# Performance work log

Measured on AMD Instinct MI355X. Metric: run time of the kernel, lower is better.

The kernel has to match this reference:

```python
import jax, jax.numpy as jnp
import numpy as np

EPS = 1e-5  # torch BatchNorm default eps
B, C, T, NOUT, NCLS = 4096, 32, 512, 16, 4


def setup_inputs() -> dict:
    key = jax.random.key(0)
    ks = jax.random.split(key, 12)
    s = lambda k, shape: jax.random.normal(k, shape, jnp.float32) * 0.05
    return {
        "de": jax.random.normal(ks[0], (B, C, T), jnp.float32),
        "adj": jax.random.normal(ks[1], (B, C, C), jnp.float32),  # unused by forward (module recomputes corr)
        "dw_w": s(ks[2], (C, 1, 3)),      # depthwise Conv1d weight [C,1,3]
        "dw_b": s(ks[3], (C,)),
        "pw_w": s(ks[4], (C, C)),          # pointwise 1x1 conv [out,in]
        "pw_b": s(ks[5], (C,)),
        "bn1_g": jnp.ones((C,), jnp.float32),
        "bn1_b": jnp.zeros((C,), jnp.float32),
        "gc_w": s(ks[6], (T, NOUT)),       # GraphConvolution weight
        "fc_w": s(ks[7], (C * NOUT, C)),   # fc62 Linear(512,32)
        "fc_b": s(ks[8], (C,)),
        "bn2_g": jnp.ones((C,), jnp.float32),
        "bn2_b": jnp.zeros((C,), jnp.float32),
        "cls_w": s(ks[9], (C, NCLS)),      # fcclass Linear(32,4)
        "cls_b": s(ks[10], (NCLS,)),
    }


def reference(de, adj, dw_w, dw_b, pw_w, pw_b, bn1_g, bn1_b, gc_w,
              fc_w, fc_b, bn2_g, bn2_b, cls_w, cls_b):
    # --- SeparableConv2d (really 1d): depthwise k=3 -> pointwise 1x1 -> BN -> relu ---
    x = jax.lax.conv_general_dilated(
        de, dw_w, window_strides=(1,), padding=[(1, 1)],
        dimension_numbers=("NCH", "OIH", "NCH"),
        feature_group_count=de.shape[1]) + dw_b[None, :, None]
    x = jnp.einsum("oc,bct->bot", pw_w, x) + pw_b[None, :, None]
    m = x.mean((0, 2), keepdims=True)
    v = x.var((0, 2), keepdims=True)  # biased, as BN normalization uses
    x = (x - m) / jnp.sqrt(v + EPS) * bn1_g[None, :, None] + bn1_b[None, :, None]
    x = jax.nn.relu(x)                       # [B, C, T]

    # --- batched Pearson corrcoef over the time axis (vectorizes the per-sample loop) ---
    xt = x.transpose(0, 2, 1)                # [B, T, C]
    Tn = xt.shape[1]
    f = (Tn - 1) / Tn
    xc = xt - xt.mean(1, keepdims=True)
    num = jnp.einsum("btn,btm->bnm", xc, xc) / Tn   # biased covariance
    var = xt.var(1, ddof=1)                         # torch var default unbiased
    den = jnp.sqrt(var[:, :, None] * var[:, None, :]) * f
    cor = num / den                          # [B, C, C]

    # --- Chebyshev graph convolution (single K term, adj = cor) + relu ---
    g = jnp.einsum("bnm,bmt->bnt", cor, x)   # message passing over channel graph
    g = jax.nn.relu(jnp.einsum("bnt,to->bno", g, gc_w))  # [B, C, 16]

    # --- fc62: Linear -> BN1d -> (dropout: identity) -> sigmoid ---
    h = g.reshape(g.shape[0], -1) @ fc_w + fc_b          # [B, 32]
    m2 = h.mean(0)
    v2 = h.var(0)
    h = (h - m2) / jnp.sqrt(v2 + EPS) * bn2_g + bn2_b
    h = jax.nn.sigmoid(h)

    return h @ cls_w + cls_b                 # [B, 4]
```

## Files before the change

### kernel.cpp

```cpp
#include <hip/hip_runtime.h>
#include <math.h>

#define BB 4096
#define CC 32
#define TT 512
#define NOUTC 16
#define EPSF 1e-5f
#define XS 520


typedef __attribute__((ext_vector_type(16))) float f32x16;
typedef __attribute__((ext_vector_type(4)))  float f32x4;
typedef __attribute__((ext_vector_type(8)))  short short8;
typedef __attribute__((ext_vector_type(4)))  unsigned int u32x4;
typedef __attribute__((ext_vector_type(4)))  float vf4;
typedef vf4 __attribute__((aligned(4))) vf4u;

__device__ __forceinline__ unsigned short f2b(float f) {
  unsigned int u = __builtin_bit_cast(unsigned int, f);
  return (unsigned short)((u + 0x7FFFu + ((u >> 16) & 1u)) >> 16);
}
__device__ __forceinline__ float blo(unsigned int u) {
  return __builtin_bit_cast(float, u << 16);
}
__device__ __forceinline__ float bhi(unsigned int u) {
  return __builtin_bit_cast(float, u & 0xFFFF0000u);
}

__device__ __forceinline__ void conv_cols(const float* __restrict__ deb,
    const float* __restrict__ dw, const float* __restrict__ db_,
    int tid, float* x1A, float* x1B) {
  int t0 = tid * 2;
  int off = (tid == 0) ? 0 : ((tid == 255) ? t0 - 2 : t0 - 1);
#pragma unroll
  for (int c = 0; c < CC; c++) {
    vf4u v = *reinterpret_cast<const vf4u*>(deb + c * TT + off);
    float vm1 = (tid == 0) ? 0.f : ((tid == 255) ? v.y : v.x);
    float v0  = (tid == 0) ? v.x : ((tid == 255) ? v.z : v.y);
    float vp1 = (tid == 0) ? v.y : ((tid == 255) ? v.w : v.z);
    float vp2 = (tid == 0) ? v.z : ((tid == 255) ? 0.f : v.w);
    float w0 = dw[c * 3], w1 = dw[c * 3 + 1], w2 = dw[c * 3 + 2], bc = db_[c];
    x1A[c] = fmaf(w0, vm1, fmaf(w1, v0, fmaf(w2, vp1, bc)));
    x1B[c] = fmaf(w0, v0, fmaf(w1, vp1, fmaf(w2, vp2, bc)));
  }
}

__global__ __launch_bounds__(256) void k1_stats(const float* __restrict__ de,
    const float* __restrict__ dw, const float* __restrict__ db_,
    const float* __restrict__ pw, const float* __restrict__ pwb,
    float* __restrict__ part, unsigned int* __restrict__ x2h, int useWs) {
  __shared__ float pr[4 * 64];
  int tid = threadIdx.x, b = blockIdx.x;
  int w = tid >> 6, lane = tid & 63;
  const float* deb = de + (size_t)b * CC * TT;
  float x1A[CC], x1B[CC];
  conv_cols(deb, dw, db_, tid, x1A, x1B);
  unsigned int* xw = x2h + (size_t)b * CC * 256;
#pragma unroll
  for (int o = 0; o < CC; o++) {
    float aA = pwb[o], aB = pwb[o];
#pragma unroll
    for (int c = 0; c < CC; c++) { float pv = pw[o * CC + c]; aA = fmaf(pv, x1A[c], aA); aB = fmaf(pv, x1B[c], aB); }
    if (useWs) xw[o * 256 + tid] = (unsigned int)f2b(aA) | ((unsigned int)f2b(aB) << 16);
    float s = aA + aB, q = fmaf(aA, aA, aB * aB);
#pragma unroll
    for (int d = 1; d < 64; d <<= 1) { s += __shfl_xor(s, d); q += __shfl_xor(q, d); }
    if (lane == 0) { pr[w * 64 + o] = s; pr[w * 64 + 32 + o] = q; }
  }
  __syncthreads();
  if (tid < 64) {
    part[(size_t)tid * BB + b] = pr[tid] + pr[64 + tid] + pr[128 + tid] + pr[192 + tid];
  }
}

__global__ void k2_bn1(const float* __restrict__ part, const float* __restrict__ g,
                       const float* __restrict__ bta, float* __restrict__ ws) {
  __shared__ float redS[256], redQ[256];
  int o = blockIdx.x, tid = threadIdx.x;
  const float* ps = part + (size_t)o * BB;
  const float* pq = part + (size_t)(CC + o) * BB;
  float s = 0, q = 0;
  for (int i = tid; i < BB; i += 256) { s += ps[i]; q += pq[i]; }
  redS[tid] = s; redQ[tid] = q;
  __syncthreads();
  for (int k = 128; k > 0; k >>= 1) {
    if (tid < k) { redS[tid] += redS[tid + k]; redQ[tid] += redQ[tid + k]; }
    __syncthreads();
  }
  if (tid == 0) {
    float N = (float)BB * (float)TT;
    float mean = redS[0] / N;
    float var = redQ[0] / N - mean * mean;
    float sc = g[o] / sqrtf(var + EPSF);
    ws[o] = sc;
    ws[32 + o] = bta[o] - mean * sc;
  }
}

__global__ __launch_bounds__(256) void k3_main(const float* __restrict__ de,
    const float* __restrict__ dw, const float* __restrict__ db_,
    const float* __restrict__ pw, const float* __restrict__ pwb,
    const float* __restrict__ ws, const float* __restrict__ gcw,
    const float* __restrict__ fcw, const float* __restrict__ fcb,
    float* __restrict__ hT, const unsigned int* __restrict__ x2h, int useWs) {
  __shared__ __align__(16) unsigned short x_s[CC * XS];
  __shared__ __align__(16) unsigned short gc_s[NOUTC * XS];
  __shared__ float gramP[2][CC * CC];
  __shared__ float zP[2][CC * NOUTC];
  __shared__ float num_s[CC * 33];
  __shared__ float red16[CC * 8];
  __shared__ float mu_s[CC], inv_s[CC];
  __shared__ float Zi_s[CC * NOUTC];
  __shared__ float g2_s[CC * NOUTC];
  __shared__ float red2[CC * 9];

  int tid = threadIdx.x, b = blockIdx.x;
  int w = tid >> 6, lane = tid & 63;
  int t0 = tid * 2;

  for (int i = tid; i < TT * NOUTC; i += 256) {
    int t = i >> 4, o = i & 15;
    gc_s[o * XS + t] = f2b(gcw[i]);
  }

  if (useWs) {
    const unsigned int* xr = x2h + (size_t)b * CC * 256;
#pragma unroll
    for (int o = 0; o < CC; o++) {
      unsigned int u = xr[o * 256 + tid];
      float sc = ws[o], sh = ws[32 + o];
      unsigned short hA = f2b(fmaxf(fmaf(blo(u), sc, sh), 0.f));
      unsigned short hB = f2b(fmaxf(fmaf(bhi(u), sc, sh), 0.f));
      *(unsigned int*)(&x_s[o * XS + t0]) = (unsigned int)hA | ((unsigned int)hB << 16);
    }
  } else {
    const float* deb = de + (size_t)b * CC * TT;
    float x1A[CC], x1B[CC];
    conv_cols(deb, dw, db_, tid, x1A, x1B);
#pragma unroll
    for (int o = 0; o < CC; o++) {
      float aA = pwb[o], aB = pwb[o];
#pragma unroll
      for (int c = 0; c < CC; c++) { float pv = pw[o * CC + c]; aA = fmaf(pv, x1A[c], aA); aB = fmaf(pv, x1B[c], aB); }
      float sc = ws[o], sh = ws[32 + o];
      unsigned short hA = f2b(fmaxf(fmaf(aA, sc, sh), 0.f));
      unsigned short hB = f2b(fmaxf(fmaf(aB, sc, sh), 0.f));
      *(unsigned int*)(&x_s[o * XS + t0]) = (unsigned int)hA | ((unsigned int)hB << 16);
    }
  }
  __syncthreads();

  {
    int c = tid >> 3, j = tid & 7;
    float s = 0.f;
#pragma unroll
    for (int it = 0; it < 8; it++) {
      u32x4 u = *reinterpret_cast<const u32x4*>(&x_s[c * XS + j * 64 + it * 8]);
#pragma unroll
      for (int k = 0; k < 4; k++) s += blo(u[k]) + bhi(u[k]);
    }
    red16[c * 8 + j] = s;
  }

  if (w < 2) {
    int m = lane & 31, kh = lane >> 5;
    f32x16 acc;
#pragma unroll
    for (int r = 0; r < 16; r++) acc[r] = 0.f;
    int kbase = w * 256 + kh * 8;
#pragma unroll
    for (int kk = 0; kk < 256; kk += 16) {
      short8 a = *(const short8*)(&x_s[m * XS + kbase + kk]);
      acc = __builtin_amdgcn_mfma_f32_32x32x16_bf16(a, a, acc, 0, 0, 0);
    }
#pragma unroll
    for (int r = 0; r < 16; r++) {
      int row = (r & 3) + 8 * (r >> 2) + 4 * kh;
      gramP[w][row * CC + m] = acc[r];
    }
  } else {
    int w2 = w - 2;
    int n16 = lane & 15, q = lane >> 4;
    f32x4 ac0, ac1;
#pragma unroll
    for (int r = 0; r < 4; r++) { ac0[r] = 0.f; ac1[r] = 0.f; }
    int kbase = w2 * 256 + q * 8;
#pragma unroll
    for (int kk = 0; kk < 256; kk += 32) {
      short8 bfr = *(const short8*)(&gc_s[n16 * XS + kbase + kk]);
      short8 af0 = *(const short8*)(&x_s[n16 * XS + kbase + kk]);
      short8 af1 = *(const short8*)(&x_s[(16 + n16) * XS + kbase + kk]);
      ac0 = __builtin_amdgcn_mfma_f32_16x16x32_bf16(af0, bfr, ac0, 0, 0, 0);
      ac1 = __builtin_amdgcn_mfma_f32_16x16x32_bf16(af1, bfr, ac1, 0, 0, 0);
    }
#pragma unroll
    for (int r = 0; r < 4; r++) {
      int row = q * 4 + r;
      zP[w2][row * NOUTC + n16] = ac0[r];
      zP[w2][(16 + row) * NOUTC + n16] = ac1[r];
    }
  }
  __syncthreads();
  if (tid < CC) {
    float s = 0.f;
#pragma unroll
    for (int j = 0; j < 8; j++) s += red16[tid * 8 + j];
    mu_s[tid] = s;
  }
  __syncthreads();
  for (int i = tid; i < CC * CC; i += 256) {
    int n = i >> 5, m = i & 31;
    num_s[n * 33 + m] = gramP[0][i] + gramP[1][i] - mu_s[n] * mu_s[m] * (1.f / (float)TT);
  }
  for (int i = tid; i < CC * NOUTC; i += 256) Zi_s[i] = zP[0][i] + zP[1][i];
  __syncthreads();
  if (tid < CC) inv_s[tid] = rsqrtf(num_s[tid * 33 + tid]);
  __syncthreads();
  for (int i = tid; i < CC * NOUTC; i += 256) {
    int n = i >> 4, o = i & 15;
    float s = 0.f;
#pragma unroll
    for (int m = 0; m < CC; m++) s = fmaf(num_s[n * 33 + m] * inv_s[m], Zi_s[m * NOUTC + o], s);
    g2_s[i] = fmaxf(s * inv_s[n], 0.f);
  }
  __syncthreads();
  {
    int j = tid & 31, ch = tid >> 5;
    float p = 0.f;
#pragma unroll
    for (int ii = 0; ii < 64; ii++) {
      int i = ch * 64 + ii;
      p = fmaf(g2_s[i], fcw[i * CC + j], p);
    }
    red2[j * 9 + ch] = p;
  }
  __syncthreads();
  if (tid < CC) {
    float h = fcb[tid];
#pragma unroll
    for (int ch = 0; ch < 8; ch++) h += red2[tid * 9 + ch];
    hT[(size_t)tid * BB + b] = h;
  }
}

__global__ void k4_bn2(const float* __restrict__ hT, const float* __restrict__ g,
                       const float* __restrict__ bta, float* __restrict__ ws) {
  __shared__ float redS[256], redQ[256];
  int j = blockIdx.x, tid = threadIdx.x;
  const float* row = hT + (size_t)j * BB;
  float s = 0, q = 0;
  for (int i = tid; i < BB; i += 256) { float v = row[i]; s += v; q = fmaf(v, v, q); }
  redS[tid] = s; redQ[tid] = q;
  __syncthreads();
  for (int k = 128; k > 0; k >>= 1) {
    if (tid < k) { redS[tid] += redS[tid + k]; redQ[tid] += redQ[tid + k]; }
    __syncthreads();
  }
  if (tid == 0) {
    float N = (float)BB;
    float mean = redS[0] / N;
    float var = redQ[0] / N - mean * mean;
    float sc = g[j] / sqrtf(var + EPSF);
    ws[64 + j] = sc;
    ws[96 + j] = bta[j] - mean * sc;
  }
}

__global__ void k5_out(const float* __restrict__ hT, const float* __restrict__ ws,
                       const float* __restrict__ clsw, const float* __restrict__ clsb,
                       float* __restrict__ out) {
  __shared__ float hs[CC * 257];
  int b0 = blockIdx.x * 256, tid = threadIdx.x;
  for (int i = tid; i < CC * 256; i += 256) {
    int j = i >> 8, bb = i & 255;
    float v = fmaf(hT[(size_t)j * BB + b0 + bb], ws[64 + j], ws[96 + j]);
    hs[j * 257 + bb] = 1.f / (1.f + expf(-v));
  }
  __syncthreads();
  float o0 = clsb[0], o1 = clsb[1], o2 = clsb[2], o3 = clsb[3];
#pragma unroll
  for (int j = 0; j < CC; j++) {
    float h = hs[j * 257 + tid];
    o0 = fmaf(h, clsw[j * 4 + 0], o0);
    o1 = fmaf(h, clsw[j * 4 + 1], o1);
    o2 = fmaf(h, clsw[j * 4 + 2], o2);
    o3 = fmaf(h, clsw[j * 4 + 3], o3);
  }
  float4* out4 = reinterpret_cast<float4*>(out);
  out4[b0 + tid] = make_float4(o0, o1, o2, o3);
}

extern "C" void kernel_launch(void* const* d_in, const int* in_sizes, int n_in,
                              void* d_out, int out_size, void* d_ws, size_t ws_size,
                              hipStream_t stream) {
  const float* de   = (const float*)d_in[0];
  const float* dw   = (const float*)d_in[2];
  const float* db_  = (const float*)d_in[3];
  const float* pw   = (const float*)d_in[4];
  const float* pwb  = (const float*)d_in[5];
  const float* bn1g = (const float*)d_in[6];
  const float* bn1b = (const float*)d_in[7];
  const float* gcw  = (const float*)d_in[8];
  const float* fcw  = (const float*)d_in[9];
  const float* fcb  = (const float*)d_in[10];
  const float* bn2g = (const float*)d_in[11];
  const float* bn2b = (const float*)d_in[12];
  const float* clsw = (const float*)d_in[13];
  const float* clsb = (const float*)d_in[14];

  float* ws   = (float*)d_ws;
  float* hT   = ws + 128;
  float* part = ws + 131200;
  unsigned int* x2h = (unsigned int*)(ws + 393344);
  float* out  = (float*)d_out;

  size_t need = 393344ull * 4ull + (size_t)BB * CC * 256 * 4;
  int useWs = (ws_size >= need) ? 1 : 0;

  k1_stats<<<BB, 256, 0, stream>>>(de, dw, db_, pw, pwb, part, x2h, useWs);
  k2_bn1<<<CC, 256, 0, stream>>>(part, bn1g, bn1b, ws);
  k3_main<<<BB, 256, 0, stream>>>(de, dw, db_, pw, pwb, ws, gcw, fcw, fcb, hT, x2h, useWs);
  k4_bn2<<<CC, 256, 0, stream>>>(hT, bn2g, bn2b, ws);
  k5_out<<<BB / 256, 256, 0, stream>>>(hT, ws, clsw, clsb, out);
}
```

Baseline: 511.5 us.

## Compute pointwise conv in k1 with split-bf16 MFMA via LDS staging

Replaces the per-thread scalar FMA loop for the 32x32 pointwise conv in k1_stats with bf16 MFMA 32x32x16 instructions. Both operands are split into hi and lo bf16 parts, and three MFMAs per k-step keep roughly fp32 accuracy. Conv outputs are staged in LDS and the results are transposed through LDS. BN statistics are then computed from the bf16-rounded values and stored as coalesced 16-byte writes. This removes a large ALU cost, but adds LDS traffic, extra barriers, and higher LDS usage that may limit occupancy. Statistics now come from rounded values, which slightly changes numerics.

Measured after the change: 521.4 us. No clear change (+1.9%).

```diff
diff --git a/kernel.cpp b/kernel.cpp
--- a/kernel.cpp
+++ b/kernel.cpp
@@ -25,6 +25,9 @@
 }
 __device__ __forceinline__ float bhi(unsigned int u) {
   return __builtin_bit_cast(float, u & 0xFFFF0000u);
+}
+__device__ __forceinline__ unsigned int pk2(float a, float b) {
+  return (unsigned int)f2b(a) | ((unsigned int)f2b(b) << 16);
 }
 
 __device__ __forceinline__ void conv_cols(const float* __restrict__ deb,
@@ -45,31 +48,116 @@
   }
 }
 
+__device__ __forceinline__ void stage_row(unsigned short* lds1, int XHo, int XLo,
+                                          int row, const float* x) {
+#pragma unroll
+  for (int cb = 0; cb < 4; cb++) {
+    u32x4 hv, lv;
+#pragma unroll
+    for (int k = 0; k < 4; k++) {
+      float a = x[cb * 8 + 2 * k], b2 = x[cb * 8 + 2 * k + 1];
+      unsigned int ua = __builtin_bit_cast(unsigned int, a);
+      unsigned int ub = __builtin_bit_cast(unsigned int, b2);
+      hv[k] = (ua >> 16) | (ub & 0xFFFF0000u);
+      float ra = a - __builtin_bit_cast(float, ua & 0xFFFF0000u);
+      float rb = b2 - __builtin_bit_cast(float, ub & 0xFFFF0000u);
+      lv[k] = pk2(ra, rb);
+    }
+    *(u32x4*)&lds1[XHo + row * 40 + cb * 8] = hv;
+    *(u32x4*)&lds1[XLo + row * 40 + cb * 8] = lv;
+  }
+}
+
 __global__ __launch_bounds__(256) void k1_stats(const float* __restrict__ de,
     const float* __restrict__ dw, const float* __restrict__ db_,
     const float* __restrict__ pw, const float* __restrict__ pwb,
     float* __restrict__ part, unsigned int* __restrict__ x2h, int useWs) {
-  __shared__ float pr[4 * 64];
+  __shared__ __align__(16) unsigned short lds1[39168];
+  const int XHo = 0, XLo = 10240, X2Bo = 20480, PWHo = 37120, PWLo = 38144;
+
   int tid = threadIdx.x, b = blockIdx.x;
-  int w = tid >> 6, lane = tid & 63;
+  int lane = tid & 63, w = tid >> 6;
+  int m31 = lane & 31, kh = lane >> 5;
+
   const float* deb = de + (size_t)b * CC * TT;
   float x1A[CC], x1B[CC];
   conv_cols(deb, dw, db_, tid, x1A, x1B);
-  unsigned int* xw = x2h + (size_t)b * CC * 256;
-#pragma unroll
-  for (int o = 0; o < CC; o++) {
-    float aA = pwb[o], aB = pwb[o];
-#pragma unroll
-    for (int c = 0; c < CC; c++) { float pv = pw[o * CC + c]; aA = fmaf(pv, x1A[c], aA); aB = fmaf(pv, x1B[c], aB); }
-    if (useWs) xw[o * 256 + tid] = (unsigned int)f2b(aA) | ((unsigned int)f2b(aB) << 16);
-    float s = aA + aB, q = fmaf(aA, aA, aB * aB);
+
+  for (int i = tid; i < CC * CC; i += 256) {
+    float v = pw[i];
+    unsigned int u = __builtin_bit_cast(unsigned int, v);
+    lds1[PWHo + i] = (unsigned short)(u >> 16);
+    float r = v - __builtin_bit_cast(float, u & 0xFFFF0000u);
+    lds1[PWLo + i] = f2b(r);
+  }
+  __syncthreads();
+
+  short8 ah[2], al[2];
+#pragma unroll
+  for (int s = 0; s < 2; s++) {
+    ah[s] = *(const short8*)&lds1[PWHo + m31 * 32 + s * 16 + kh * 8];
+    al[s] = *(const short8*)&lds1[PWLo + m31 * 32 + s * 16 + kh * 8];
+  }
+  float pbv[16];
+#pragma unroll
+  for (int r = 0; r < 16; r++) pbv[r] = pwb[(r & 3) + 8 * (r >> 2) + 4 * kh];
+
+#pragma unroll
+  for (int h = 0; h < 2; h++) {
+    if ((tid >> 7) == h) {
+      int lr = 2 * (tid & 127);
+      stage_row(lds1, XHo, XLo, lr, x1A);
+      stage_row(lds1, XHo, XLo, lr + 1, x1B);
+    }
+    __syncthreads();
+
+#pragma unroll
+    for (int i = 0; i < 2; i++) {
+      int wt = w * 2 + i;
+      f32x16 acc;
+#pragma unroll
+      for (int r = 0; r < 16; r++) acc[r] = 0.f;
+      int rowb = wt * 32 + m31;
+#pragma unroll
+      for (int s = 0; s < 2; s++) {
+        short8 bh = *(const short8*)&lds1[XHo + rowb * 40 + s * 16 + kh * 8];
+        short8 bl = *(const short8*)&lds1[XLo + rowb * 40 + s * 16 + kh * 8];
+        acc = __builtin_amdgcn_mfma_f32_32x32x16_bf16(ah[s], bh, acc, 0, 0, 0);
+        acc = __builtin_amdgcn_mfma_f32_32x32x16_bf16(ah[s], bl, acc, 0, 0, 0);
+        acc = __builtin_amdgcn_mfma_f32_32x32x16_bf16(al[s], bh, acc, 0, 0, 0);
+      }
+      int t = h * 256 + wt * 32 + m31;
+#pragma unroll
+      for (int pr = 0; pr < 8; pr++) {
+        int o0 = ((2 * pr) & 3) + 8 * (pr >> 1) + 4 * kh;
+        unsigned int p = pk2(acc[2 * pr] + pbv[2 * pr], acc[2 * pr + 1] + pbv[2 * pr + 1]);
+        lds1[X2Bo + o0 * 520 + t] = (unsigned short)(p & 0xFFFFu);
+        lds1[X2Bo + (o0 + 1) * 520 + t] = (unsigned short)(p >> 16);
+      }
+    }
+    __syncthreads();
+  }
+
+  unsigned int* xw = x2h + (size_t)b * (CC * 256);
+  int L = tid & 63;
+#pragma unroll
+  for (int it = 0; it < 8; it++) {
+    int o = it * 4 + w;
+    u32x4 v = *(const u32x4*)&lds1[X2Bo + o * 520 + L * 8];
+    float s = 0.f, q = 0.f;
+#pragma unroll
+    for (int k = 0; k < 4; k++) {
+      float a = blo(v[k]), c2 = bhi(v[k]);
+      s += a + c2;
+      q = fmaf(a, a, fmaf(c2, c2, q));
+    }
 #pragma unroll
     for (int d = 1; d < 64; d <<= 1) { s += __shfl_xor(s, d); q += __shfl_xor(q, d); }
-    if (lane == 0) { pr[w * 64 + o] = s; pr[w * 64 + 32 + o] = q; }
-  }
-  __syncthreads();
-  if (tid < 64) {
-    part[(size_t)tid * BB + b] = pr[tid] + pr[64 + tid] + pr[128 + tid] + pr[192 + tid];
+    if (L == 0) {
+      part[(size_t)o * BB + b] = s;
+      part[(size_t)(32 + o) * BB + b] = q;
+    }
+    if (useWs) *(u32x4*)(xw + (size_t)(it * 256 + tid) * 4) = v;
   }
 }
 
```
